# Performance work log

Hardware: AMD Instinct MI355X
Metric: run time of the kernel (lower is better)

Reference implementation:

```python
import jax, jax.numpy as jnp
import numpy as np
import math

C = 512          # in_planes
H = 8            # num_heads
D = C // H       # head_dim = 64
EPS = 1e-12      # torch F.normalize eps


def _l2norm(x):
    # F.normalize(x, dim=-1): x / max(||x||_2, eps)
    n = jnp.sqrt(jnp.sum(x * x, axis=-1, keepdims=True))
    return x / jnp.maximum(n, EPS)


def setup_inputs() -> dict:
    key = jax.random.key(0)
    ks = jax.random.split(key, 8)
    q = jax.random.normal(ks[0], (8, 8, 256, C), dtype=jnp.float32)
    kv = jax.random.normal(ks[1], (8, 8, 512, C), dtype=jnp.float32)
    s = 0.02
    Wq = jax.random.normal(ks[2], (C, C), dtype=jnp.float32) * s
    bq = jax.random.normal(ks[3], (C,), dtype=jnp.float32) * s
    Wkv = jax.random.normal(ks[4], (2 * C, C), dtype=jnp.float32) * s
    bkv = jax.random.normal(ks[5], (2 * C,), dtype=jnp.float32) * s
    Wm = jax.random.normal(ks[6], (C, C), dtype=jnp.float32) * s
    bm = jax.random.normal(ks[7], (C,), dtype=jnp.float32) * s
    return {"q": q, "kv": kv, "Wq": Wq, "bq": bq, "Wkv": Wkv, "bkv": bkv, "Wm": Wm, "bm": bm}


def reference(q, kv, Wq, bq, Wkv, bkv, Wm, bm):
    b, t, lq, c = q.shape
    lk = kv.shape[2]
    shortcut = q

    # Q projection -> (b,t,h,lq,d), L2-normalized over d
    qh = (q @ Wq.T + bq).reshape(b, t, lq, H, D)
    qh = _l2norm(jnp.moveaxis(qh, 3, 2))  # (b,t,h,lq,d)

    # KV projection -> (b,t,2h,lk,d); first H heads = k, last H = v
    kvh = (kv @ Wkv.T + bkv).reshape(b, t, lk, 2 * H, D)
    kvh = jnp.moveaxis(kvh, 3, 2)          # (b,t,2h,lk,d)
    kh = _l2norm(kvh[:, :, :H])            # (b,t,h,lk,d)
    vh = _l2norm(kvh[:, :, H:])            # (b,t,h,lk,d)

    # cosine attention
    att = jnp.einsum('bthqd,bthkd->bthqk', qh, kh) / math.sqrt(D)
    att = jax.nn.softmax(att, axis=-1)
    x = jnp.einsum('bthqk,bthkd->bthqd', att, vh)  # (b,t,h,lq,d)

    # merge heads, output projection, residual
    x = jnp.moveaxis(x, 2, 3).reshape(b, t, lq, c)
    return x @ Wm.T + bm + shortcut
```

## Files before the change

### kernel.cpp

```cpp
#include <hip/hip_runtime.h>
#include <hip/hip_bf16.h>

using bf = __bf16;
typedef __attribute__((ext_vector_type(8))) __bf16 bf16x8;
typedef __attribute__((ext_vector_type(4))) float f32x4;

#define MFMA(a, b, c) __builtin_amdgcn_mfma_f32_16x16x32_bf16((a), (b), (c), 0, 0, 0)
#define GLL16(g, s)                                                         \
    __builtin_amdgcn_global_load_lds(                                       \
        (const __attribute__((address_space(1))) void*)(g),                 \
        (__attribute__((address_space(3))) void*)(s), 16, 0, 0)

static __device__ __forceinline__ void cvt_one(const float* __restrict__ s,
                                               bf* __restrict__ d, int i)
{
    const f32x4 a = ((const f32x4*)s)[2 * i];
    const f32x4 b = ((const f32x4*)s)[2 * i + 1];
    bf16x8 r;
#pragma unroll
    for (int k = 0; k < 4; ++k) { r[k] = (bf)a[k]; r[4 + k] = (bf)b[k]; }
    ((bf16x8*)d)[i] = r;
}

__global__ __launch_bounds__(256) void cvt2(const float* __restrict__ s1, bf* __restrict__ d1, int n1,
                                            const float* __restrict__ s2, bf* __restrict__ d2, int n2)
{
    int i = blockIdx.x * 256 + threadIdx.x;
    if (i < n1) { cvt_one(s1, d1, i); return; }
    i -= n1;
    if (i < n2) cvt_one(s2, d2, i);
}

__global__ __launch_bounds__(256) void cvt3(const float* __restrict__ s1, bf* __restrict__ d1, int n1,
                                            const float* __restrict__ s2, bf* __restrict__ d2, int n2,
                                            const float* __restrict__ s3, bf* __restrict__ d3, int n3)
{
    int i = blockIdx.x * 256 + threadIdx.x;
    if (i < n1) { cvt_one(s1, d1, i); return; }
    i -= n1;
    if (i < n2) { cvt_one(s2, d2, i); return; }
    i -= n2;
    if (i < n3) cvt_one(s3, d3, i);
}

template <int EPI, int GH, int LGR>
__global__ __launch_bounds__(256) void gemm128(
    const bf* __restrict__ A, const bf* __restrict__ W,
    const float* __restrict__ bias, const float* __restrict__ res,
    void* __restrict__ Cout, int M, int N, int K)
{
    __shared__ __attribute__((aligned(16))) bf As[128 * 32];
    __shared__ __attribute__((aligned(16))) bf Bs[128 * 32];

    const int lane = threadIdx.x & 63;
    const int wave = threadIdx.x >> 6;
    const int lm = lane & 15;
    const int quad = lane >> 4;
    const int row0 = blockIdx.x * 128, col0 = blockIdx.y * 128;
    const int wrow = (wave >> 1) * 64, wcol = (wave & 1) * 64;

    const int sr = lane >> 2;
    const int sc = (lane & 3) * 8;
    const bf* Ag = A + (size_t)(row0 + wave * 32 + sr) * K + sc;
    const bf* Wg = W + (size_t)(col0 + wave * 32 + sr) * K + sc;
    bf* AsW = As + wave * 1024;
    bf* BsW = Bs + wave * 1024;

    f32x4 acc[4][4] = {};

    for (int k0 = 0; k0 < K; k0 += 32) {
        GLL16(Ag + k0, AsW);
        GLL16(Ag + (size_t)16 * K + k0, AsW + 512);
        GLL16(Wg + k0, BsW);
        GLL16(Wg + (size_t)16 * K + k0, BsW + 512);
        __syncthreads();

        bf16x8 a[4], b[4];
#pragma unroll
        for (int i = 0; i < 4; ++i)
            a[i] = *(const bf16x8*)(As + (wrow + i * 16 + lm) * 32 + quad * 8);
#pragma unroll
        for (int j = 0; j < 4; ++j)
            b[j] = *(const bf16x8*)(Bs + (wcol + j * 16 + lm) * 32 + quad * 8);
#pragma unroll
        for (int i = 0; i < 4; ++i)
#pragma unroll
            for (int j = 0; j < 4; ++j)
                acc[i][j] = MFMA(a[i], b[j], acc[i][j]);
        __syncthreads();
    }

    float bv[4];
#pragma unroll
    for (int j = 0; j < 4; ++j) bv[j] = bias[col0 + wcol + j * 16 + lm];

    if (EPI == 0) {
        bf* C = (bf*)Cout;
        const int g = (col0 + wcol) >> 6;
#pragma unroll
        for (int i = 0; i < 4; ++i) {
#pragma unroll
            for (int rg = 0; rg < 4; ++rg) {
                float v[4];
                float ss = 0.f;
#pragma unroll
                for (int j = 0; j < 4; ++j) {
                    const float x = acc[i][j][rg] + bv[j];
                    v[j] = x;
                    ss += x * x;
                }
                ss += __shfl_xor(ss, 1, 64);
                ss += __shfl_xor(ss, 2, 64);
                ss += __shfl_xor(ss, 4, 64);
                ss += __shfl_xor(ss, 8, 64);
                const float inv = 1.0f / fmaxf(sqrtf(ss), 1e-12f);
                const int row = row0 + wrow + i * 16 + quad * 4 + rg;
                const int bt = row >> LGR;
                const int rl = row & ((1 << LGR) - 1);
                bf* Cr = C + (((size_t)(bt * GH + g) << LGR) + rl) * 64;
#pragma unroll
                for (int j = 0; j < 4; ++j)
                    Cr[j * 16 + lm] = (bf)(v[j] * inv);
            }
        }
    } else {
        float* C = (float*)Cout;
#pragma unroll
        for (int i = 0; i < 4; ++i) {
#pragma unroll
            for (int rg = 0; rg < 4; ++rg) {
                const int row = row0 + wrow + i * 16 + quad * 4 + rg;
#pragma unroll
                for (int j = 0; j < 4; ++j) {
                    const size_t idx = (size_t)row * N + col0 + wcol + j * 16 + lm;
                    C[idx] = acc[i][j][rg] + bv[j] + res[idx];
                }
            }
        }
    }
}

__global__ __launch_bounds__(256, 4) void attn(
    const bf* __restrict__ qn, const bf* __restrict__ kvn, bf* __restrict__ X)
{
    __shared__ __attribute__((aligned(16))) bf Kt[128 * 72];
    __shared__ __attribute__((aligned(16))) bf Vt[64 * 136];
    __shared__ __attribute__((aligned(16))) bf Ps[4][16 * 40];

    const int qb = blockIdx.x >> 9;
    const int rb = blockIdx.x & 511;
    const int bt = rb >> 3;
    const int h = rb & 7;
    const int tid = threadIdx.x;
    const int lane = tid & 63;
    const int wave = tid >> 6;
    const int lm = lane & 15;
    const int quad = lane >> 4;

    const bf* qh = qn + ((size_t)(bt * 8 + h) * 256 + qb * 128) * 64;
    const bf* kh = kvn + (size_t)(bt * 16 + h) * 512 * 64;
    const bf* vh = kvn + (size_t)(bt * 16 + 8 + h) * 512 * 64;

    const int srow = tid >> 1;
    const int sseg = (tid & 1) * 32;

    f32x4 o[2][4] = {};
    float sum[2][4] = {};
    bf* Pw = &Ps[wave][0];

    for (int t = 0; t < 4; ++t) {
        {
            const bf* kr = kh + (size_t)(t * 128 + srow) * 64 + sseg;
            bf* kd = Kt + srow * 72 + sseg;
#pragma unroll
            for (int j = 0; j < 4; ++j)
                *(bf16x8*)(kd + j * 8) = *(const bf16x8*)(kr + j * 8);

            const bf* vr = vh + (size_t)(t * 128 + srow) * 64 + sseg;
            bf16x8 vv[4];
#pragma unroll
            for (int j = 0; j < 4; ++j) vv[j] = *(const bf16x8*)(vr + j * 8);
#pragma unroll
            for (int j = 0; j < 4; ++j)
#pragma unroll
                for (int e = 0; e < 8; ++e)
                    Vt[(sseg + j * 8 + e) * 136 + srow] = vv[j][e];
        }
        __syncthreads();

#pragma unroll
        for (int c = 0; c < 2; ++c) {
            const int r0 = wave * 32 + c * 16;
            const bf* qp = qh + (size_t)(r0 + lm) * 64 + quad * 8;
            const bf16x8 a0 = *(const bf16x8*)qp;
            const bf16x8 a1 = *(const bf16x8*)(qp + 32);

            f32x4 s[8];
#pragma unroll
            for (int nt = 0; nt < 8; ++nt) {
                const bf16x8 k0 = *(const bf16x8*)(&Kt[(nt * 16 + lm) * 72 + quad * 8]);
                const bf16x8 k1 = *(const bf16x8*)(&Kt[(nt * 16 + lm) * 72 + 32 + quad * 8]);
                f32x4 z = {};
                z = MFMA(a0, k0, z);
                s[nt] = MFMA(a1, k1, z);
            }

            for (int ntp = 0; ntp < 4; ++ntp) {
#pragma unroll
                for (int tt = 0; tt < 2; ++tt)
#pragma unroll
                    for (int rr = 0; rr < 4; ++rr) {
                        const float e = __expf(s[ntp * 2 + tt][rr] * 0.125f);
                        sum[c][rr] += e;
                        Pw[(quad * 4 + rr) * 40 + tt * 16 + lm] = (bf)e;
                    }
                const bf16x8 ap = *(const bf16x8*)(&Pw[lm * 40 + quad * 8]);
#pragma unroll
                for (int dt = 0; dt < 4; ++dt) {
                    const bf16x8 bv = *(const bf16x8*)(&Vt[(dt * 16 + lm) * 136 + ntp * 32 + quad * 8]);
                    o[c][dt] = MFMA(ap, bv, o[c][dt]);
                }
            }
        }
        __syncthreads();
    }

#pragma unroll
    for (int c = 0; c < 2; ++c) {
        float inv[4];
#pragma unroll
        for (int rr = 0; rr < 4; ++rr) {
            float sm = sum[c][rr];
            sm += __shfl_xor(sm, 1, 64);
            sm += __shfl_xor(sm, 2, 64);
            sm += __shfl_xor(sm, 4, 64);
            sm += __shfl_xor(sm, 8, 64);
            inv[rr] = 1.0f / sm;
        }
        bf* Xp = X + ((size_t)bt * 256 + qb * 128 + wave * 32 + c * 16) * 512 + h * 64;
#pragma unroll
        for (int dt = 0; dt < 4; ++dt)
#pragma unroll
            for (int rr = 0; rr < 4; ++rr)
                Xp[(size_t)(quad * 4 + rr) * 512 + dt * 16 + lm] = (bf)(o[c][dt][rr] * inv[rr]);
    }
}

extern "C" void kernel_launch(void* const* d_in, const int* in_sizes, int n_in,
                              void* d_out, int out_size, void* d_ws, size_t ws_size,
                              hipStream_t stream)
{
    const float* q   = (const float*)d_in[0];
    const float* kv  = (const float*)d_in[1];
    const float* Wq  = (const float*)d_in[2];
    const float* bq  = (const float*)d_in[3];
    const float* Wkv = (const float*)d_in[4];
    const float* bkv = (const float*)d_in[5];
    const float* Wm  = (const float*)d_in[6];
    const float* bm  = (const float*)d_in[7];
    float* out = (float*)d_out;

    char* ws = (char*)d_ws;
    bf* kvb = (bf*)ws;
    bf* kvn = (bf*)(ws + (size_t)(32 << 20));
    bf* wqb = (bf*)ws;
    bf* wmb = (bf*)(ws + (size_t)(16 << 20));
    bf* X   = (bf*)ws;
    char* dob = (char*)d_out;
    bf* wkvb = (bf*)dob;
    bf* qb   = (bf*)dob;
    bf* qn   = (bf*)(dob + (size_t)(16 << 20));

    cvt2<<<dim3(8448), 256, 0, stream>>>(kv, kvb, 2097152, Wkv, wkvb, 65536);
    gemm128<0, 16, 9><<<dim3(256, 8), 256, 0, stream>>>(kvb, wkvb, bkv, nullptr, kvn, 32768, 1024, 512);
    cvt3<<<dim3(4352), 256, 0, stream>>>(q, qb, 1048576, Wq, wqb, 32768, Wm, wmb, 32768);
    gemm128<0, 8, 8><<<dim3(128, 4), 256, 0, stream>>>(qb, wqb, bq, nullptr, qn, 16384, 512, 512);
    attn<<<dim3(1024), 256, 0, stream>>>(qn, kvn, X);
    gemm128<1, 0, 0><<<dim3(128, 4), 256, 0, stream>>>(X, wmb, bm, q, out, 16384, 512, 512);
}
```

Before: 283.3 us.

## Use 256x256-tile pipelined GEMM with fused L2-norm for Q/KV projections

Adds a new 512-thread GEMM kernel with 256x256 output tiles, double-buffered direct-to-LDS loads, XOR-swizzled shared memory and barrier-phased MFMA scheduling with priority hints. The epilogue applies bias, per-head L2 normalization and the head-major scatter. It replaces the 128-tile GEMM for the KV and Q projections. The goal is more data reuse per tile and better overlap of loads with MFMA. The cost is 128 KB of dynamic LDS and fewer blocks per CU, and only 128 blocks for the Q projection, which may underfill the GPU.

```diff
diff --git a/kernel.cpp b/kernel.cpp
--- a/kernel.cpp
+++ b/kernel.cpp
@@ -140,6 +140,158 @@
     }
 }
 
+template <int GH, int LGR>
+__global__ __launch_bounds__(512, 2) void gemm256(
+    const bf* __restrict__ A, const bf* __restrict__ W,
+    const float* __restrict__ bias, bf* __restrict__ C,
+    int M, int N, int K)
+{
+    extern __shared__ __attribute__((aligned(16))) char smem[];
+    char* Asm = smem;
+    char* Bsm = smem + 65536;
+
+    const int tid = threadIdx.x;
+    const int lane = tid & 63;
+    const int lm = lane & 15;
+    const int quad = lane >> 4;
+    const int wave = tid >> 6;
+    const int wm = wave >> 2;
+    const int wn = wave & 3;
+    const int row0 = blockIdx.x * 256, col0 = blockIdx.y * 256;
+    const int NT = K >> 6;
+
+    const int trow = tid >> 3;
+    const int tslot = (tid & 7) ^ (trow & 7);
+    const bf* Ath = A + (size_t)(row0 + trow) * K + tslot * 8;
+    const bf* Wth = W + (size_t)(col0 + trow) * K + tslot * 8;
+
+    const char* aBase = Asm + wm * 16384 + lm * 128;
+    const char* bBase = Bsm + (wn >> 1) * 16384 + ((wn & 1) * 64 + lm) * 128;
+    const int skz0 = ((quad ^ (lm & 7)) << 4);
+    const int skz1 = (((4 + quad) ^ (lm & 7)) << 4);
+
+    f32x4 acc[8][4] = {};
+
+    auto stA = [&](int kt) {
+        const int bo = (kt & 1) * 32768;
+#pragma unroll
+        for (int h = 0; h < 2; ++h)
+#pragma unroll
+            for (int s = 0; s < 2; ++s)
+                GLL16(Ath + (size_t)(h * 128 + s * 64) * K + kt * 64,
+                      Asm + bo + h * 16384 + s * 8192 + tid * 16);
+    };
+    auto stB = [&](int kt) {
+        const int bo = (kt & 1) * 32768;
+#pragma unroll
+        for (int h = 0; h < 2; ++h)
+#pragma unroll
+            for (int s = 0; s < 2; ++s)
+                GLL16(Wth + (size_t)(h * 128 + s * 64) * K + kt * 64,
+                      Bsm + bo + h * 16384 + s * 8192 + tid * 16);
+    };
+
+#define LOADA(bo, mh, kk)                                                     \
+    _Pragma("unroll")                                                         \
+    for (int mm = 0; mm < 4; ++mm)                                            \
+        a[mm] = *(const bf16x8*)(aBase + (bo) + ((mh) * 4 + mm) * 2048        \
+                                 + ((kk) ? skz1 : skz0));
+#define LOADB(bo, kk)                                                         \
+    _Pragma("unroll")                                                         \
+    for (int j = 0; j < 4; ++j)                                               \
+        b[j] = *(const bf16x8*)(bBase + (bo) + j * 2048                       \
+                                + ((kk) ? skz1 : skz0));
+#define PH_OPEN()                                                             \
+    __builtin_amdgcn_s_barrier();                                             \
+    asm volatile("s_waitcnt lgkmcnt(0)" ::: "memory");                        \
+    __builtin_amdgcn_s_setprio(1)
+#define MM16(mh)                                                              \
+    _Pragma("unroll")                                                         \
+    for (int mm = 0; mm < 4; ++mm)                                            \
+        _Pragma("unroll")                                                     \
+        for (int j = 0; j < 4; ++j)                                           \
+            acc[(mh) * 4 + mm][j] = MFMA(a[mm], b[j], acc[(mh) * 4 + mm][j]);
+#define PH_CLOSE()                                                            \
+    __builtin_amdgcn_s_setprio(0);                                            \
+    __builtin_amdgcn_s_barrier()
+
+    stB(0); stA(0); stB(1);
+    asm volatile("s_waitcnt vmcnt(4)" ::: "memory");
+    __builtin_amdgcn_s_barrier();
+
+    for (int it = 0; it < NT; it += 2) {
+        const int more = (it + 2 < NT);
+        bf16x8 a[4], b[4];
+
+        LOADA(0, 0, 0) LOADB(0, 0) stA(it + 1);
+        PH_OPEN(); MM16(0) PH_CLOSE();
+
+        LOADA(0, 1, 0)
+        PH_OPEN(); MM16(1) PH_CLOSE();
+
+        LOADA(0, 0, 1) LOADB(0, 1)
+        PH_OPEN(); MM16(0) PH_CLOSE();
+
+        LOADA(0, 1, 1) if (more) stB(it + 2);
+        PH_OPEN(); MM16(1)
+        __builtin_amdgcn_s_setprio(0);
+        if (more) { asm volatile("s_waitcnt vmcnt(4)" ::: "memory"); }
+        else      { asm volatile("s_waitcnt vmcnt(0)" ::: "memory"); }
+        __builtin_amdgcn_s_barrier();
+
+        LOADA(32768, 0, 0) LOADB(32768, 0) if (more) stA(it + 2);
+        PH_OPEN(); MM16(0) PH_CLOSE();
+
+        LOADA(32768, 1, 0)
+        PH_OPEN(); MM16(1) PH_CLOSE();
+
+        LOADA(32768, 0, 1) LOADB(32768, 1)
+        PH_OPEN(); MM16(0) PH_CLOSE();
+
+        LOADA(32768, 1, 1) if (more) stB(it + 3);
+        PH_OPEN(); MM16(1)
+        __builtin_amdgcn_s_setprio(0);
+        if (more) { asm volatile("s_waitcnt vmcnt(4)" ::: "memory"); }
+        __builtin_amdgcn_s_barrier();
+    }
+#undef LOADA
+#undef LOADB
+#undef PH_OPEN
+#undef MM16
+#undef PH_CLOSE
+
+    float bv[4];
+#pragma unroll
+    for (int j = 0; j < 4; ++j) bv[j] = bias[col0 + wn * 64 + j * 16 + lm];
+    const int g = (col0 + wn * 64) >> 6;
+#pragma unroll
+    for (int m = 0; m < 8; ++m) {
+#pragma unroll
+        for (int rg = 0; rg < 4; ++rg) {
+            float v[4];
+            float ss = 0.f;
+#pragma unroll
+            for (int j = 0; j < 4; ++j) {
+                const float x = acc[m][j][rg] + bv[j];
+                v[j] = x;
+                ss += x * x;
+            }
+            ss += __shfl_xor(ss, 1, 64);
+            ss += __shfl_xor(ss, 2, 64);
+            ss += __shfl_xor(ss, 4, 64);
+            ss += __shfl_xor(ss, 8, 64);
+            const float inv = 1.0f / fmaxf(sqrtf(ss), 1e-12f);
+            const int row = row0 + wm * 128 + m * 16 + quad * 4 + rg;
+            const int bt = row >> LGR;
+            const int rl = row & ((1 << LGR) - 1);
+            bf* Cr = C + (((size_t)(bt * GH + g) << LGR) + rl) * 64;
+#pragma unroll
+            for (int j = 0; j < 4; ++j)
+                Cr[j * 16 + lm] = (bf)(v[j] * inv);
+        }
+    }
+}
+
 __global__ __launch_bounds__(256, 4) void attn(
     const bf* __restrict__ qn, const bf* __restrict__ kvn, bf* __restrict__ X)
 {
@@ -271,10 +423,17 @@
     bf* qb   = (bf*)dob;
     bf* qn   = (bf*)(dob + (size_t)(16 << 20));
 
+    {
+        auto k0 = gemm256<16, 9>;
+        auto k1 = gemm256<8, 8>;
+        (void)hipFuncSetAttribute((const void*)k0, hipFuncAttributeMaxDynamicSharedMemorySize, 131072);
+        (void)hipFuncSetAttribute((const void*)k1, hipFuncAttributeMaxDynamicSharedMemorySize, 131072);
+    }
+
     cvt2<<<dim3(8448), 256, 0, stream>>>(kv, kvb, 2097152, Wkv, wkvb, 65536);
-    gemm128<0, 16, 9><<<dim3(256, 8), 256, 0, stream>>>(kvb, wkvb, bkv, nullptr, kvn, 32768, 1024, 512);
+    gemm256<16, 9><<<dim3(128, 4), 512, 131072, stream>>>(kvb, wkvb, bkv, kvn, 32768, 1024, 512);
     cvt3<<<dim3(4352), 256, 0, stream>>>(q, qb, 1048576, Wq, wqb, 32768, Wm, wmb, 32768);
-    gemm128<0, 8, 8><<<dim3(128, 4), 256, 0, stream>>>(qb, wqb, bq, nullptr, qn, 16384, 512, 512);
+    gemm256<8, 8><<<dim3(64, 2), 512, 131072, stream>>>(qb, wqb, bq, qn, 16384, 512, 512);
     attn<<<dim3(1024), 256, 0, stream>>>(qn, kvn, X);
     gemm128<1, 0, 0><<<dim3(128, 4), 256, 0, stream>>>(X, wmb, bm, q, out, 16384, 512, 512);
 }
```

Result: no change. 287.3 us (+1.4%).

## Use 256x256-tile GEMM kernel for KV projection with fused L2-norm epilogue

Applied to the files above, without the earlier changes.

Adds a new gemm256 kernel with 512 threads and 256x256 output tiles, double-buffered LDS fed by global_load_lds, and raised wave priority around the MFMA blocks. It replaces the 128x128 gemm128 launch for the KV projection. Larger tiles double operand reuse per LDS load and halve the number of blocks, which cuts global traffic. The cost is 64KB of dynamic shared memory and a large accumulator register footprint, which may limit occupancy; the grid also drops to 512 blocks.

```diff
diff --git a/kernel.cpp b/kernel.cpp
--- a/kernel.cpp
+++ b/kernel.cpp
@@ -140,6 +140,113 @@
     }
 }
 
+template <int GH, int LGR>
+__global__ __launch_bounds__(512, 4) void gemm256(
+    const bf* __restrict__ A, const bf* __restrict__ W,
+    const float* __restrict__ bias, bf* __restrict__ C,
+    int M, int N, int K)
+{
+    extern __shared__ __attribute__((aligned(16))) char smem[];
+    char* Asm = smem;
+    char* Bsm = smem + 32768;
+
+    const int tid = threadIdx.x;
+    const int lane = tid & 63;
+    const int lm = lane & 15;
+    const int quad = lane >> 4;
+    const int wave = tid >> 6;
+    const int wm = wave >> 2;
+    const int wn = wave & 3;
+    const int row0 = blockIdx.x * 256, col0 = blockIdx.y * 256;
+    const int NT = K >> 5;
+
+    const int trow = tid >> 2;
+    const int sswz = (tid & 3) ^ (trow & 3);
+    const bf* Ath = A + (size_t)(row0 + trow) * K + sswz * 8;
+    const bf* Wth = W + (size_t)(col0 + trow) * K + sswz * 8;
+
+    const char* aBase = Asm + wm * 8192;
+    const char* bBase = Bsm + wn * 4096;
+    const int sk = ((quad ^ (lm & 3)) << 4);
+
+    f32x4 acc[8][4] = {};
+
+    auto stage = [&](int kt) {
+        const int bo = (kt & 1) * 16384;
+        const int ko = kt * 32;
+        GLL16(Ath + ko, Asm + bo + tid * 16);
+        GLL16(Ath + (size_t)128 * K + ko, Asm + bo + 8192 + tid * 16);
+        GLL16(Wth + ko, Bsm + bo + tid * 16);
+        GLL16(Wth + (size_t)128 * K + ko, Bsm + bo + 8192 + tid * 16);
+    };
+
+    stage(0);
+    asm volatile("s_waitcnt vmcnt(0)" ::: "memory");
+    __builtin_amdgcn_s_barrier();
+
+    for (int t = 0; t < NT; ++t) {
+        if (t + 1 < NT) stage(t + 1);
+        const int bo = (t & 1) * 16384;
+        bf16x8 a[4], b[4];
+#pragma unroll
+        for (int j = 0; j < 4; ++j)
+            b[j] = *(const bf16x8*)(bBase + bo + (j * 16 + lm) * 64 + sk);
+#pragma unroll
+        for (int mm = 0; mm < 4; ++mm)
+            a[mm] = *(const bf16x8*)(aBase + bo + (mm * 16 + lm) * 64 + sk);
+        __builtin_amdgcn_s_setprio(1);
+#pragma unroll
+        for (int mm = 0; mm < 4; ++mm)
+#pragma unroll
+            for (int j = 0; j < 4; ++j)
+                acc[mm][j] = MFMA(a[mm], b[j], acc[mm][j]);
+        __builtin_amdgcn_s_setprio(0);
+#pragma unroll
+        for (int mm = 0; mm < 4; ++mm)
+            a[mm] = *(const bf16x8*)(aBase + bo + ((4 + mm) * 16 + lm) * 64 + sk);
+        __builtin_amdgcn_s_setprio(1);
+#pragma unroll
+        for (int mm = 0; mm < 4; ++mm)
+#pragma unroll
+            for (int j = 0; j < 4; ++j)
+                acc[4 + mm][j] = MFMA(a[mm], b[j], acc[4 + mm][j]);
+        __builtin_amdgcn_s_setprio(0);
+        asm volatile("s_waitcnt vmcnt(0)" ::: "memory");
+        __builtin_amdgcn_s_barrier();
+    }
+
+    float bv[4];
+#pragma unroll
+    for (int j = 0; j < 4; ++j) bv[j] = bias[col0 + wn * 64 + j * 16 + lm];
+    const int g = (col0 + wn * 64) >> 6;
+#pragma unroll
+    for (int m = 0; m < 8; ++m) {
+#pragma unroll
+        for (int rg = 0; rg < 4; ++rg) {
+            float v[4];
+            float ss = 0.f;
+#pragma unroll
+            for (int j = 0; j < 4; ++j) {
+                const float x = acc[m][j][rg] + bv[j];
+                v[j] = x;
+                ss += x * x;
+            }
+            ss += __shfl_xor(ss, 1, 64);
+            ss += __shfl_xor(ss, 2, 64);
+            ss += __shfl_xor(ss, 4, 64);
+            ss += __shfl_xor(ss, 8, 64);
+            const float inv = 1.0f / fmaxf(sqrtf(ss), 1e-12f);
+            const int row = row0 + wm * 128 + m * 16 + quad * 4 + rg;
+            const int bt = row >> LGR;
+            const int rl = row & ((1 << LGR) - 1);
+            bf* Cr = C + (((size_t)(bt * GH + g) << LGR) + rl) * 64;
+#pragma unroll
+            for (int j = 0; j < 4; ++j)
+                Cr[j * 16 + lm] = (bf)(v[j] * inv);
+        }
+    }
+}
+
 __global__ __launch_bounds__(256, 4) void attn(
     const bf* __restrict__ qn, const bf* __restrict__ kvn, bf* __restrict__ X)
 {
@@ -271,8 +378,13 @@
     bf* qb   = (bf*)dob;
     bf* qn   = (bf*)(dob + (size_t)(16 << 20));
 
+    {
+        auto k0 = gemm256<16, 9>;
+        (void)hipFuncSetAttribute((const void*)k0, hipFuncAttributeMaxDynamicSharedMemorySize, 65536);
+    }
+
     cvt2<<<dim3(8448), 256, 0, stream>>>(kv, kvb, 2097152, Wkv, wkvb, 65536);
-    gemm128<0, 16, 9><<<dim3(256, 8), 256, 0, stream>>>(kvb, wkvb, bkv, nullptr, kvn, 32768, 1024, 512);
+    gemm256<16, 9><<<dim3(128, 4), 512, 65536, stream>>>(kvb, wkvb, bkv, kvn, 32768, 1024, 512);
     cvt3<<<dim3(4352), 256, 0, stream>>>(q, qb, 1048576, Wq, wqb, 32768, Wm, wmb, 32768);
     gemm128<0, 8, 8><<<dim3(128, 4), 256, 0, stream>>>(qb, wqb, bq, nullptr, qn, 16384, 512, 512);
     attn<<<dim3(1024), 256, 0, stream>>>(qn, kvn, X);
```

Result: slower. 532.0 us (+87.8%).
